# Optimization experiments

Hardware: AMD Instinct MI355X
Metric: run time of the kernel (lower is better)

## Reference

```python
import jax, jax.numpy as jnp
import numpy as np


def _local_conv2d(x, w, b):
    """Untied (locally connected) conv, stride 1, VALID.
    x: (B, C, H, W); w: (1, O, C, Ho, Wo, k*k); b: (1, O, Ho, Wo) or None.
    Matches torch: x.unfold(2,k).unfold(3,k) -> (B,C,Ho,Wo,k,k) flattened (k*k),
    then (x[:,None] * w).sum([2,-1]) + b.
    """
    B, C, H, W = x.shape
    Ho, Wo = w.shape[3], w.shape[4]
    kh = H - Ho + 1
    kw = W - Wo + 1
    # patches: (B, C*kh*kw, Ho, Wo), feature dim ordered (C, kh, kw) — same as torch unfold
    patches = jax.lax.conv_general_dilated_patches(x, (kh, kw), (1, 1), 'VALID')
    patches = patches.reshape(B, C, kh * kw, Ho, Wo)
    out = jnp.einsum('bckhw,ochwk->bohw', patches, w[0])
    if b is not None:
        out = out + b
    return out


def _maxpool2(x):
    return jax.lax.reduce_window(x, -jnp.inf, jax.lax.max,
                                 (1, 1, 2, 2), (1, 1, 2, 2), 'VALID')


def setup_inputs() -> dict:
    key = jax.random.key(0)
    ks = jax.random.split(key, 11)
    B, C, H, W = 1024, 3, 32, 32
    s = lambda k, shape, fan: jax.random.normal(k, shape, jnp.float32) * np.sqrt(2.0 / fan)
    return {
        'x': jax.random.normal(ks[0], (B, C, H, W), jnp.float32),
        'w1': s(ks[1], (1, 6, 3, 28, 28, 25), 3 * 25),
        'b1': s(ks[2], (1, 6, 28, 28), 28 * 28) ,
        'w2': s(ks[3], (1, 16, 6, 10, 10, 25), 6 * 25),
        'b2': s(ks[4], (1, 16, 10, 10), 10 * 10),
        'w3': s(ks[5], (1, 120, 16, 1, 1, 25), 16 * 25),
        'b3': s(ks[6], (1, 120, 1, 1), 1),
        'fc2_w': s(ks[7], (84, 120), 120),
        'fc2_b': jnp.zeros((84,), jnp.float32),
        'fc3_w': s(ks[8], (10, 84), 84),
        'fc3_b': jnp.zeros((10,), jnp.float32),
    }


def reference(x, w1, b1, w2, b2, w3, b3, fc2_w, fc2_b, fc3_w, fc3_b):
    h = _maxpool2(jax.nn.relu(_local_conv2d(x, w1, b1)))   # (B,6,14,14)
    h = _maxpool2(jax.nn.relu(_local_conv2d(h, w2, b2)))   # (B,16,5,5)
    h = jax.nn.relu(_local_conv2d(h, w3, b3))              # (B,120,1,1)
    h = h.reshape(h.shape[0], -1)                          # (B,120)
    h = jax.nn.relu(h @ fc2_w.T + fc2_b)                   # (B,84)
    return h @ fc3_w.T + fc3_b                             # (B,10)
```

## Files before the change

### kernel.cpp

```cpp
#include <hip/hip_runtime.h>
#include <math.h>

#define NB 1024

__global__ __launch_bounds__(256) void k_transpose(const float* __restrict__ x,
                                                   float* __restrict__ xT) {
  __shared__ float tile[64][65];
  const int c0 = blockIdx.x * 64;
  const int b0 = blockIdx.y * 64;
  const int tx = threadIdx.x & 63;
  const int ty = threadIdx.x >> 6;
#pragma unroll
  for (int r = 0; r < 16; ++r) {
    const int bb = r * 4 + ty;
    tile[bb][tx] = x[(size_t)(b0 + bb) * 3072 + c0 + tx];
  }
  __syncthreads();
#pragma unroll
  for (int r = 0; r < 16; ++r) {
    const int cc = r * 4 + ty;
    xT[(size_t)(c0 + cc) * NB + b0 + tx] = tile[tx][cc];
  }
}

__global__ __launch_bounds__(128) void k_conv1(const float* __restrict__ xT,
                                               const float* __restrict__ w1,
                                               const float* __restrict__ b1,
                                               float* __restrict__ h1) {
  const int w = blockIdx.x;
  const int xcd = w & 7, kk = w >> 3;
  const int bg = xcd >> 1;
  const int pos = (xcd & 1) * 98 + kk;
  const int ph = pos / 14, pw = pos % 14;
  const int b = bg * 256 + threadIdx.x * 2;

  __shared__ __align__(16) float wL[72 * 28];
  __shared__ float bL[24];
  for (int t = threadIdx.x; t < 72 * 25; t += 128) {
    const int chunk = t / 25, p = t - chunk * 25;
    const int o = chunk / 12, rem = chunk - o * 12;
    const int c = rem >> 2, i = (rem >> 1) & 1, j = rem & 1;
    wL[chunk * 28 + p] =
        w1[((size_t)((o * 3 + c) * 28 + (2 * ph + i)) * 28 + (2 * pw + j)) * 25 + p];
  }
  if (threadIdx.x < 24) {
    const int o = threadIdx.x >> 2, i = (threadIdx.x >> 1) & 1, j = threadIdx.x & 1;
    bL[threadIdx.x] = b1[(size_t)(o * 28 + (2 * ph + i)) * 28 + (2 * pw + j)];
  }
  __syncthreads();

  float2 acc[6][2][2];
#pragma unroll
  for (int o = 0; o < 6; ++o)
#pragma unroll
    for (int i = 0; i < 2; ++i)
#pragma unroll
      for (int j = 0; j < 2; ++j) { acc[o][i][j].x = 0.f; acc[o][i][j].y = 0.f; }

  for (int c = 0; c < 3; ++c) {
    float2 xw[6][6];
#pragma unroll
    for (int dh = 0; dh < 6; ++dh)
#pragma unroll
      for (int dw = 0; dw < 6; ++dw)
        xw[dh][dw] = *reinterpret_cast<const float2*>(
            &xT[((size_t)(c * 32 + (2 * ph + dh)) * 32 + (2 * pw + dw)) * NB + b]);
#pragma unroll
    for (int o = 0; o < 6; ++o)
#pragma unroll
      for (int i = 0; i < 2; ++i)
#pragma unroll
        for (int j = 0; j < 2; ++j) {
          const float* wp = &wL[((o * 3 + c) * 4 + i * 2 + j) * 28];
#pragma unroll
          for (int p = 0; p < 25; ++p) {
            const float wv = wp[p];
            const float2 xv = xw[i + p / 5][j + p % 5];
            acc[o][i][j].x = fmaf(xv.x, wv, acc[o][i][j].x);
            acc[o][i][j].y = fmaf(xv.y, wv, acc[o][i][j].y);
          }
        }
  }

#pragma unroll
  for (int o = 0; o < 6; ++o) {
    float2 v[2][2];
#pragma unroll
    for (int i = 0; i < 2; ++i)
#pragma unroll
      for (int j = 0; j < 2; ++j) {
        const float bias = bL[o * 4 + i * 2 + j];
        v[i][j].x = fmaxf(acc[o][i][j].x + bias, 0.f);
        v[i][j].y = fmaxf(acc[o][i][j].y + bias, 0.f);
      }
    float2 m;
    m.x = fmaxf(fmaxf(v[0][0].x, v[0][1].x), fmaxf(v[1][0].x, v[1][1].x));
    m.y = fmaxf(fmaxf(v[0][0].y, v[0][1].y), fmaxf(v[1][0].y, v[1][1].y));
    *reinterpret_cast<float2*>(&h1[((size_t)(o * 14 + ph) * 14 + pw) * NB + b]) = m;
  }
}

__global__ __launch_bounds__(128) void k_conv2(const float* __restrict__ h1,
                                               const float* __restrict__ w2,
                                               const float* __restrict__ b2,
                                               float* __restrict__ h2) {
  const int w = blockIdx.x;
  const int xcd = w & 7, kk = w >> 3;
  const int bg = xcd >> 1;
  const int unit = (xcd & 1) * 100 + kk;
  const int og = unit / 25;
  const int pos = unit % 25;
  const int ph = pos / 5, pw = pos % 5;
  const int b = bg * 256 + threadIdx.x * 2;

  __shared__ __align__(16) float wL[48 * 28];
  __shared__ float bL[8];
  for (int t = threadIdx.x; t < 48 * 25; t += 128) {
    const int chunk = t / 25, p = t - chunk * 25;
    const int oo = chunk / 24, rem = chunk - oo * 24;
    const int c = rem >> 2, i = (rem >> 1) & 1, j = rem & 1;
    const int o = og * 2 + oo;
    wL[chunk * 28 + p] =
        w2[((size_t)((o * 6 + c) * 10 + (2 * ph + i)) * 10 + (2 * pw + j)) * 25 + p];
  }
  if (threadIdx.x < 8) {
    const int oo = threadIdx.x >> 2, i = (threadIdx.x >> 1) & 1, j = threadIdx.x & 1;
    const int o = og * 2 + oo;
    bL[threadIdx.x] = b2[(size_t)(o * 10 + (2 * ph + i)) * 10 + (2 * pw + j)];
  }
  __syncthreads();

  float2 acc[2][2][2];
#pragma unroll
  for (int oo = 0; oo < 2; ++oo)
#pragma unroll
    for (int i = 0; i < 2; ++i)
#pragma unroll
      for (int j = 0; j < 2; ++j) { acc[oo][i][j].x = 0.f; acc[oo][i][j].y = 0.f; }

  for (int c = 0; c < 6; ++c) {
    float2 xw[6][6];
#pragma unroll
    for (int dh = 0; dh < 6; ++dh)
#pragma unroll
      for (int dw = 0; dw < 6; ++dw)
        xw[dh][dw] = *reinterpret_cast<const float2*>(
            &h1[((size_t)(c * 14 + (2 * ph + dh)) * 14 + (2 * pw + dw)) * NB + b]);
#pragma unroll
    for (int oo = 0; oo < 2; ++oo)
#pragma unroll
      for (int i = 0; i < 2; ++i)
#pragma unroll
        for (int j = 0; j < 2; ++j) {
          const float* wp = &wL[((oo * 6 + c) * 4 + i * 2 + j) * 28];
#pragma unroll
          for (int p = 0; p < 25; ++p) {
            const float wv = wp[p];
            const float2 xv = xw[i + p / 5][j + p % 5];
            acc[oo][i][j].x = fmaf(xv.x, wv, acc[oo][i][j].x);
            acc[oo][i][j].y = fmaf(xv.y, wv, acc[oo][i][j].y);
          }
        }
  }

#pragma unroll
  for (int oo = 0; oo < 2; ++oo) {
    const int o = og * 2 + oo;
    float2 v[2][2];
#pragma unroll
    for (int i = 0; i < 2; ++i)
#pragma unroll
      for (int j = 0; j < 2; ++j) {
        const float bias = bL[oo * 4 + i * 2 + j];
        v[i][j].x = fmaxf(acc[oo][i][j].x + bias, 0.f);
        v[i][j].y = fmaxf(acc[oo][i][j].y + bias, 0.f);
      }
    float2 m;
    m.x = fmaxf(fmaxf(v[0][0].x, v[0][1].x), fmaxf(v[1][0].x, v[1][1].x));
    m.y = fmaxf(fmaxf(v[0][0].y, v[0][1].y), fmaxf(v[1][0].y, v[1][1].y));
    *reinterpret_cast<float2*>(&h2[((size_t)(o * 5 + ph) * 5 + pw) * NB + b]) = m;
  }
}

__global__ __launch_bounds__(128) void k_conv3(const float* __restrict__ h2,
                                               const float* __restrict__ w3,
                                               const float* __restrict__ b3,
                                               float* __restrict__ h3) {
  const int w = blockIdx.x;
  const int xcd = w & 7, k2 = w >> 3;
  const int bg = xcd >> 1;
  const int o = ((xcd & 1) * 30 + k2) * 2;
  const int b = bg * 256 + threadIdx.x * 2;

  __shared__ __align__(16) float wL[2][400];
  for (int t = threadIdx.x; t < 800; t += 128) {
    const int oo = t / 400, p = t - oo * 400;
    wL[oo][p] = w3[(size_t)(o + oo) * 400 + p];
  }
  __syncthreads();

  float2 a00 = {0.f, 0.f}, a01 = {0.f, 0.f}, a10 = {0.f, 0.f}, a11 = {0.f, 0.f};
#pragma unroll 4
  for (int k = 0; k < 400; k += 2) {
    const float2 x0 = *reinterpret_cast<const float2*>(&h2[(size_t)(k + 0) * NB + b]);
    const float2 x1 = *reinterpret_cast<const float2*>(&h2[(size_t)(k + 1) * NB + b]);
    const float w00 = wL[0][k], w01 = wL[0][k + 1];
    const float w10 = wL[1][k], w11 = wL[1][k + 1];
    a00.x = fmaf(x0.x, w00, a00.x); a00.y = fmaf(x0.y, w00, a00.y);
    a01.x = fmaf(x1.x, w01, a01.x); a01.y = fmaf(x1.y, w01, a01.y);
    a10.x = fmaf(x0.x, w10, a10.x); a10.y = fmaf(x0.y, w10, a10.y);
    a11.x = fmaf(x1.x, w11, a11.x); a11.y = fmaf(x1.y, w11, a11.y);
  }
  float2 r0, r1;
  r0.x = fmaxf(a00.x + a01.x + b3[o], 0.f);
  r0.y = fmaxf(a00.y + a01.y + b3[o], 0.f);
  r1.x = fmaxf(a10.x + a11.x + b3[o + 1], 0.f);
  r1.y = fmaxf(a10.y + a11.y + b3[o + 1], 0.f);
  *reinterpret_cast<float2*>(&h3[(size_t)o * NB + b]) = r0;
  *reinterpret_cast<float2*>(&h3[(size_t)(o + 1) * NB + b]) = r1;
}

__global__ __launch_bounds__(256) void k_fctail(const float* __restrict__ h3,
                                                const float* __restrict__ fc2w,
                                                const float* __restrict__ fc2b,
                                                const float* __restrict__ fc3w,
                                                const float* __restrict__ fc3b,
                                                float* __restrict__ out) {
  const int b0 = blockIdx.x * 16;
  const int tid = threadIdx.x;
  __shared__ float h3L[120 * 16];
  __shared__ float h4L[84 * 16];

  for (int t = tid; t < 120 * 16; t += 256) {
    const int k = t >> 4, bb = t & 15;
    h3L[t] = h3[(size_t)k * NB + b0 + bb];
  }
  __syncthreads();

  const int bb = tid & 15;
  {
    const int jbase = tid >> 4;
#pragma unroll
    for (int jr = 0; jr < 6; ++jr) {
      const int j = jbase + jr * 16;
      if (j < 84) {
        const float* __restrict__ wp = fc2w + (size_t)j * 120;
        float a0 = 0.f, a1 = 0.f;
#pragma unroll
        for (int k = 0; k < 120; k += 2) {
          a0 = fmaf(h3L[(k + 0) * 16 + bb], wp[k + 0], a0);
          a1 = fmaf(h3L[(k + 1) * 16 + bb], wp[k + 1], a1);
        }
        h4L[j * 16 + bb] = fmaxf(a0 + a1 + fc2b[j], 0.f);
      }
    }
  }
  __syncthreads();

  if (tid < 160) {
    const int i = tid >> 4;
    const float* __restrict__ wp = fc3w + (size_t)i * 84;
    float a0 = 0.f, a1 = 0.f;
#pragma unroll
    for (int j = 0; j < 84; j += 2) {
      a0 = fmaf(h4L[(j + 0) * 16 + bb], wp[j + 0], a0);
      a1 = fmaf(h4L[(j + 1) * 16 + bb], wp[j + 1], a1);
    }
    out[(size_t)(b0 + bb) * 10 + i] = a0 + a1 + fc3b[i];
  }
}

extern "C" void kernel_launch(void* const* d_in, const int* in_sizes, int n_in,
                              void* d_out, int out_size, void* d_ws, size_t ws_size,
                              hipStream_t stream) {
  const float* x    = (const float*)d_in[0];
  const float* w1   = (const float*)d_in[1];
  const float* b1   = (const float*)d_in[2];
  const float* w2   = (const float*)d_in[3];
  const float* b2   = (const float*)d_in[4];
  const float* w3   = (const float*)d_in[5];
  const float* b3   = (const float*)d_in[6];
  const float* fc2w = (const float*)d_in[7];
  const float* fc2b = (const float*)d_in[8];
  const float* fc3w = (const float*)d_in[9];
  const float* fc3b = (const float*)d_in[10];
  float* out = (float*)d_out;

  float* ws = (float*)d_ws;
  float* xT = ws;
  float* h1 = xT + 3145728;
  float* h2 = h1 + 1204224;
  float* h3 = h2 + 409600;

  k_transpose<<<dim3(48, 16), 256, 0, stream>>>(x, xT);
  k_conv1<<<dim3(784), 128, 0, stream>>>(xT, w1, b1, h1);
  k_conv2<<<dim3(800), 128, 0, stream>>>(h1, w2, b2, h2);
  k_conv3<<<dim3(240), 128, 0, stream>>>(h2, w3, b3, h3);
  k_fctail<<<dim3(64), 256, 0, stream>>>(h3, fc2w, fc2b, fc3w, fc3b, out);
}
```

Baseline: 166.0 us.

## Fuse conv3 and fully-connected tail into one per-batch-tile kernel

Replaces the separate conv3 and FC-tail kernels with one kernel. Each block handles 4 batch items: it stages h2 in LDS, computes the 120 conv3 outputs in chunks of 16 with a 4-way split-K reduction, then runs fc2 and fc3 from LDS-staged weights. This removes one launch and the h3 round trip through global memory. In exchange, every block re-reads the full w3 and fc2 weights and reuses them across only 4 batch items, which raises L2 traffic and adds many barriers per block. The last chunk covers outputs 120-127, so it reads w3 and b3 past the end of the buffers; those results land in LDS slots that fc2 never reads.

```diff
diff --git a/kernel.cpp b/kernel.cpp
--- a/kernel.cpp
+++ b/kernel.cpp
@@ -182,91 +182,90 @@
   }
 }
 
-__global__ __launch_bounds__(128) void k_conv3(const float* __restrict__ h2,
-                                               const float* __restrict__ w3,
-                                               const float* __restrict__ b3,
-                                               float* __restrict__ h3) {
-  const int w = blockIdx.x;
-  const int xcd = w & 7, k2 = w >> 3;
-  const int bg = xcd >> 1;
-  const int o = ((xcd & 1) * 30 + k2) * 2;
-  const int b = bg * 256 + threadIdx.x * 2;
-
-  __shared__ __align__(16) float wL[2][400];
-  for (int t = threadIdx.x; t < 800; t += 128) {
-    const int oo = t / 400, p = t - oo * 400;
-    wL[oo][p] = w3[(size_t)(o + oo) * 400 + p];
-  }
-  __syncthreads();
-
-  float2 a00 = {0.f, 0.f}, a01 = {0.f, 0.f}, a10 = {0.f, 0.f}, a11 = {0.f, 0.f};
+__global__ __launch_bounds__(256) void k_tail(const float* __restrict__ h2,
+                                              const float* __restrict__ w3,
+                                              const float* __restrict__ b3,
+                                              const float* __restrict__ fc2w,
+                                              const float* __restrict__ fc2b,
+                                              const float* __restrict__ fc3w,
+                                              const float* __restrict__ fc3b,
+                                              float* __restrict__ out) {
+  __shared__ __align__(16) float smem[11232];
+  float* h3L = smem;
+  float* h4L = smem + 480;
+  float* scr = smem + 816;
+  const int tid = threadIdx.x;
+  const int b0 = blockIdx.x * 4;
+
+  float* h2L = scr;
+  float* w3c = scr + 1600;
+  float* red = scr + 8064;
+  for (int idx = tid; idx < 1600; idx += 256) {
+    const int k = idx >> 2, bb = idx & 3;
+    h2L[idx] = h2[(size_t)k * NB + b0 + bb];
+  }
+
+  const int lane = tid & 63;
+  const int kseg = tid >> 6;
+  const int oo = lane >> 2;
+  const int bb = lane & 3;
+
+  for (int c3 = 0; c3 < 8; ++c3) {
+    __syncthreads();
+    const int o0 = c3 * 16;
+    for (int idx = tid; idx < 6400; idx += 256) {
+      const int r = idx / 400;
+      w3c[r * 404 + (idx - r * 400)] = w3[(size_t)o0 * 400 + idx];
+    }
+    __syncthreads();
+    float acc = 0.f;
+    const int kbase = kseg * 100;
+    const float* wrow = &w3c[oo * 404];
 #pragma unroll 4
-  for (int k = 0; k < 400; k += 2) {
-    const float2 x0 = *reinterpret_cast<const float2*>(&h2[(size_t)(k + 0) * NB + b]);
-    const float2 x1 = *reinterpret_cast<const float2*>(&h2[(size_t)(k + 1) * NB + b]);
-    const float w00 = wL[0][k], w01 = wL[0][k + 1];
-    const float w10 = wL[1][k], w11 = wL[1][k + 1];
-    a00.x = fmaf(x0.x, w00, a00.x); a00.y = fmaf(x0.y, w00, a00.y);
-    a01.x = fmaf(x1.x, w01, a01.x); a01.y = fmaf(x1.y, w01, a01.y);
-    a10.x = fmaf(x0.x, w10, a10.x); a10.y = fmaf(x0.y, w10, a10.y);
-    a11.x = fmaf(x1.x, w11, a11.x); a11.y = fmaf(x1.y, w11, a11.y);
-  }
-  float2 r0, r1;
-  r0.x = fmaxf(a00.x + a01.x + b3[o], 0.f);
-  r0.y = fmaxf(a00.y + a01.y + b3[o], 0.f);
-  r1.x = fmaxf(a10.x + a11.x + b3[o + 1], 0.f);
-  r1.y = fmaxf(a10.y + a11.y + b3[o + 1], 0.f);
-  *reinterpret_cast<float2*>(&h3[(size_t)o * NB + b]) = r0;
-  *reinterpret_cast<float2*>(&h3[(size_t)(o + 1) * NB + b]) = r1;
-}
-
-__global__ __launch_bounds__(256) void k_fctail(const float* __restrict__ h3,
-                                                const float* __restrict__ fc2w,
-                                                const float* __restrict__ fc2b,
-                                                const float* __restrict__ fc3w,
-                                                const float* __restrict__ fc3b,
-                                                float* __restrict__ out) {
-  const int b0 = blockIdx.x * 16;
-  const int tid = threadIdx.x;
-  __shared__ float h3L[120 * 16];
-  __shared__ float h4L[84 * 16];
-
-  for (int t = tid; t < 120 * 16; t += 256) {
-    const int k = t >> 4, bb = t & 15;
-    h3L[t] = h3[(size_t)k * NB + b0 + bb];
-  }
-  __syncthreads();
-
-  const int bb = tid & 15;
-  {
-    const int jbase = tid >> 4;
-#pragma unroll
-    for (int jr = 0; jr < 6; ++jr) {
-      const int j = jbase + jr * 16;
-      if (j < 84) {
-        const float* __restrict__ wp = fc2w + (size_t)j * 120;
-        float a0 = 0.f, a1 = 0.f;
-#pragma unroll
-        for (int k = 0; k < 120; k += 2) {
-          a0 = fmaf(h3L[(k + 0) * 16 + bb], wp[k + 0], a0);
-          a1 = fmaf(h3L[(k + 1) * 16 + bb], wp[k + 1], a1);
-        }
-        h4L[j * 16 + bb] = fmaxf(a0 + a1 + fc2b[j], 0.f);
-      }
-    }
-  }
-  __syncthreads();
-
-  if (tid < 160) {
-    const int i = tid >> 4;
-    const float* __restrict__ wp = fc3w + (size_t)i * 84;
+    for (int k = kbase; k < kbase + 100; ++k)
+      acc = fmaf(wrow[k], h2L[k * 4 + bb], acc);
+    red[tid] = acc;
+    __syncthreads();
+    if (tid < 64) {
+      const int o = o0 + (tid >> 2);
+      const float s = (red[tid] + red[tid + 64]) + (red[tid + 128] + red[tid + 192]);
+      h3L[o * 4 + (tid & 3)] = fmaxf(s + b3[o], 0.f);
+    }
+  }
+  __syncthreads();
+
+  float* fc2wL = scr;
+  for (int idx = tid; idx < 84 * 120; idx += 256) {
+    const int j = idx / 120;
+    fc2wL[j * 124 + (idx - j * 120)] = fc2w[idx];
+  }
+  __syncthreads();
+  for (int item = tid; item < 84 * 4; item += 256) {
+    const int j = item >> 2, b2i = item & 3;
+    const float* wrow = &fc2wL[j * 124];
     float a0 = 0.f, a1 = 0.f;
-#pragma unroll
+#pragma unroll 4
+    for (int k = 0; k < 120; k += 2) {
+      a0 = fmaf(wrow[k + 0], h3L[(k + 0) * 4 + b2i], a0);
+      a1 = fmaf(wrow[k + 1], h3L[(k + 1) * 4 + b2i], a1);
+    }
+    h4L[j * 4 + b2i] = fmaxf(a0 + a1 + fc2b[j], 0.f);
+  }
+  __syncthreads();
+
+  float* fc3wL = scr;
+  for (int idx = tid; idx < 840; idx += 256) fc3wL[idx] = fc3w[idx];
+  __syncthreads();
+  if (tid < 40) {
+    const int i = tid >> 2, b2i = tid & 3;
+    const float* wrow = &fc3wL[i * 84];
+    float a0 = 0.f, a1 = 0.f;
+#pragma unroll 4
     for (int j = 0; j < 84; j += 2) {
-      a0 = fmaf(h4L[(j + 0) * 16 + bb], wp[j + 0], a0);
-      a1 = fmaf(h4L[(j + 1) * 16 + bb], wp[j + 1], a1);
-    }
-    out[(size_t)(b0 + bb) * 10 + i] = a0 + a1 + fc3b[i];
+      a0 = fmaf(wrow[j + 0], h4L[(j + 0) * 4 + b2i], a0);
+      a1 = fmaf(wrow[j + 1], h4L[(j + 1) * 4 + b2i], a1);
+    }
+    out[(size_t)(b0 + b2i) * 10 + i] = a0 + a1 + fc3b[i];
   }
 }
 
@@ -290,11 +289,9 @@
   float* xT = ws;
   float* h1 = xT + 3145728;
   float* h2 = h1 + 1204224;
-  float* h3 = h2 + 409600;
 
   k_transpose<<<dim3(48, 16), 256, 0, stream>>>(x, xT);
   k_conv1<<<dim3(784), 128, 0, stream>>>(xT, w1, b1, h1);
   k_conv2<<<dim3(800), 128, 0, stream>>>(h1, w2, b2, h2);
-  k_conv3<<<dim3(240), 128, 0, stream>>>(h2, w3, b3, h3);
-  k_fctail<<<dim3(64), 256, 0, stream>>>(h3, fc2w, fc2b, fc3w, fc3b, out);
-}
+  k_tail<<<dim3(256), 256, 0, stream>>>(h2, w3, b3, fc2w, fc2b, fc3w, fc3b, out);
+}
```

After: 165.3 us. About the same (-0.4%).
